# Performance work log

Measured on AMD Instinct MI355X. Metric: run time of the kernel, lower is better.

## Reference

```python
import jax, jax.numpy as jnp
import numpy as np

B, H, S, D = 4, 16, 2048, 64

def setup_inputs() -> dict:
    key = jax.random.key(0)
    kq, kk, kv = jax.random.split(key, 3)
    q = jax.random.normal(kq, (B, H, S, D), dtype=jnp.float32)
    k = jax.random.normal(kk, (B, H, S, D), dtype=jnp.float32)
    v = jax.random.normal(kv, (B, H, S, D), dtype=jnp.float32)
    # broadcastable causal mask: True = attend
    mask = jnp.tril(jnp.ones((S, S), dtype=bool))[None, None, :, :]
    return {"q": q, "k": k, "v": v, "mask": mask}

def reference(q, k, v, mask):
    # qk = einsum('... q d, ... k d -> ... q k'); mask -> -inf; softmax(qk/sqrt(d_k)); @ v
    scale = 1.0 / jnp.sqrt(jnp.asarray(q.shape[-1], q.dtype))
    scores = jnp.einsum('bhqd,bhkd->bhqk', q, k)
    scores = jnp.where(mask, scores, -jnp.inf) * scale  # -inf * scale stays -inf
    attn = jax.nn.softmax(scores, axis=-1)
    return jnp.einsum('bhqk,bhkd->bhqd', attn, v)
```

## Files before the change

kernel.cpp:

```cpp
#include <hip/hip_runtime.h>
#include <hip/hip_bf16.h>


#define SEQ 2048
#define HD  64

typedef __attribute__((ext_vector_type(8))) short short8;
typedef __attribute__((ext_vector_type(4))) float f32x4;

__device__ __forceinline__ short f2bf(float f) {
    union { float f; unsigned u; } x; x.f = f;
    unsigned r = x.u + 0x7fff + ((x.u >> 16) & 1);
    return (short)(r >> 16);
}

__device__ __forceinline__ short8 pack8(f32x4 a, f32x4 b, float s) {
    short8 t;
    t[0]=f2bf(a[0]*s); t[1]=f2bf(a[1]*s); t[2]=f2bf(a[2]*s); t[3]=f2bf(a[3]*s);
    t[4]=f2bf(b[0]*s); t[5]=f2bf(b[1]*s); t[6]=f2bf(b[2]*s); t[7]=f2bf(b[3]*s);
    return t;
}

#define KLD 72
#define VLD 40
#define ELD 68

__global__ __launch_bounds__(256, 4) void sdpa_kernel(
    const float* __restrict__ Q, const float* __restrict__ K,
    const float* __restrict__ V, float* __restrict__ O)
{
    __shared__ __align__(16) char smraw[4 * 16 * ELD * 4];
    short* Klds = (short*)smraw;
    short* Vlds = (short*)(smraw + 4608);

    const int bx = blockIdx.x;
    const int qt = 31 - (bx >> 6);
    const int bh = bx & 63;
    const int qbase = qt * 64;

    const int tid  = threadIdx.x;
    const int lane = tid & 63;
    const int w    = tid >> 6;
    const int g    = lane >> 4;
    const int r16  = lane & 15;
    const int wq   = qbase + w * 16;
    const int qrow = wq + r16;

    short8 qf[2];
    {
        const float* qp = Q + (size_t)(bh * SEQ + qrow) * HD + 8 * g;
        #pragma unroll
        for (int c = 0; c < 2; ++c) {
            f32x4 a = *(const f32x4*)(qp + c * 32);
            f32x4 b = *(const f32x4*)(qp + c * 32 + 4);
            qf[c] = pack8(a, b, 0.125f);
        }
    }

    f32x4 oacc[4] = {};
    float mrun = -1e30f, lrun = 0.0f;

    const int nkvb = (qbase + 64) >> 5;
    for (int kvb = 0; kvb < nkvb; ++kvb) {
        const int kvbase = kvb << 5;

        {
            const int kvo = tid >> 3;
            const int dc  = (tid & 7) * 8;
            const float* kp = K + (size_t)(bh * SEQ + kvbase + kvo) * HD + dc;
            f32x4 a = *(const f32x4*)kp;
            f32x4 b = *(const f32x4*)(kp + 4);
            const int p = 16 * ((kvo >> 2) & 1) + 4 * (kvo >> 3) + (kvo & 3);
            *(short8*)&Klds[p * KLD + dc] = pack8(a, b, 1.0f);
        }
        {
            const int kvo = tid & 31;
            const int dc  = (tid >> 5) * 8;
            const float* vp = V + (size_t)(bh * SEQ + kvbase + kvo) * HD + dc;
            f32x4 a = *(const f32x4*)vp;
            f32x4 b = *(const f32x4*)(vp + 4);
            Vlds[(dc + 0) * VLD + kvo] = f2bf(a[0]);
            Vlds[(dc + 1) * VLD + kvo] = f2bf(a[1]);
            Vlds[(dc + 2) * VLD + kvo] = f2bf(a[2]);
            Vlds[(dc + 3) * VLD + kvo] = f2bf(a[3]);
            Vlds[(dc + 4) * VLD + kvo] = f2bf(b[0]);
            Vlds[(dc + 5) * VLD + kvo] = f2bf(b[1]);
            Vlds[(dc + 6) * VLD + kvo] = f2bf(b[2]);
            Vlds[(dc + 7) * VLD + kvo] = f2bf(b[3]);
        }
        __syncthreads();

        if (kvbase <= wq + 15) {
            f32x4 sa[2];
            #pragma unroll
            for (int t = 0; t < 2; ++t) {
                f32x4 acc = {};
                #pragma unroll
                for (int c = 0; c < 2; ++c) {
                    short8 kf = *(const short8*)&Klds[(t * 16 + r16) * KLD + c * 32 + 8 * g];
                    acc = __builtin_amdgcn_mfma_f32_16x16x32_bf16(kf, qf[c], acc, 0, 0, 0);
                }
                sa[t] = acc;
            }
            if (kvbase + 31 > wq) {
                #pragma unroll
                for (int t = 0; t < 2; ++t)
                    #pragma unroll
                    for (int r = 0; r < 4; ++r) {
                        int kv = kvbase + 8 * g + 4 * t + r;
                        if (kv > qrow) sa[t][r] = -1e30f;
                    }
            }
            float mloc = sa[0][0];
            #pragma unroll
            for (int t = 0; t < 2; ++t)
                #pragma unroll
                for (int r = 0; r < 4; ++r) mloc = fmaxf(mloc, sa[t][r]);
            mloc = fmaxf(mloc, __shfl_xor(mloc, 16));
            mloc = fmaxf(mloc, __shfl_xor(mloc, 32));
            float mnew = fmaxf(mrun, mloc);
            float alpha = __expf(mrun - mnew);
            float ls = 0.0f;
            #pragma unroll
            for (int t = 0; t < 2; ++t)
                #pragma unroll
                for (int r = 0; r < 4; ++r) {
                    float p = __expf(sa[t][r] - mnew);
                    sa[t][r] = p; ls += p;
                }
            ls += __shfl_xor(ls, 16);
            ls += __shfl_xor(ls, 32);
            lrun = lrun * alpha + ls;
            mrun = mnew;
            short8 pf;
            pf[0] = f2bf(sa[0][0]); pf[1] = f2bf(sa[0][1]);
            pf[2] = f2bf(sa[0][2]); pf[3] = f2bf(sa[0][3]);
            pf[4] = f2bf(sa[1][0]); pf[5] = f2bf(sa[1][1]);
            pf[6] = f2bf(sa[1][2]); pf[7] = f2bf(sa[1][3]);
            #pragma unroll
            for (int dt = 0; dt < 4; ++dt) {
                f32x4 t2 = oacc[dt] * alpha;
                short8 vf = *(const short8*)&Vlds[(dt * 16 + r16) * VLD + 8 * g];
                oacc[dt] = __builtin_amdgcn_mfma_f32_16x16x32_bf16(vf, pf, t2, 0, 0, 0);
            }
        }
        __syncthreads();
    }

    const float inv = 1.0f / lrun;
    float* ep = (float*)smraw + w * (16 * ELD);
    #pragma unroll
    for (int dt = 0; dt < 4; ++dt)
        #pragma unroll
        for (int r = 0; r < 4; ++r)
            ep[r16 * ELD + dt * 16 + 4 * g + r] = oacc[dt][r] * inv;
    __syncthreads();

    const int qr = lane >> 2;
    const int cb = (lane & 3) * 16;
    const float* eprow = ep + qr * ELD + cb;
    float* op = O + (size_t)(bh * SEQ + wq + qr) * HD + cb;
    #pragma unroll
    for (int i = 0; i < 4; ++i)
        *(f32x4*)(op + 4 * i) = *(const f32x4*)(eprow + 4 * i);
}

extern "C" void kernel_launch(void* const* d_in, const int* in_sizes, int n_in,
                              void* d_out, int out_size, void* d_ws, size_t ws_size,
                              hipStream_t stream) {
    (void)in_sizes; (void)n_in; (void)out_size; (void)d_ws; (void)ws_size;
    const float* q = (const float*)d_in[0];
    const float* k = (const float*)d_in[1];
    const float* v = (const float*)d_in[2];
    float* o = (float*)d_out;
    sdpa_kernel<<<dim3(64 * 32), dim3(256), 0, stream>>>(q, k, v, o);
}
```

Measured before the change: 226.1 us.

## Enlarge attention tiles to 128 queries and 64 keys with swizzled LDS

Each workgroup now covers 128 query rows (two 16-row subtiles per wave) and 64-key blocks instead of 64/32. Every K and V fragment loaded from LDS therefore feeds two MFMAs, and there are fewer block iterations and barriers. LDS now uses XOR-swizzled layouts in place of padding, and bf16 conversion packs two values per word. Softmax uses exp2 with the log2e factor folded into the Q scale. The output is written straight from registers rather than staged through LDS. The cost is higher register pressure (launch bounds lowered to 2), half as many workgroups, and coarser causal-tile load imbalance.

```diff
diff --git a/kernel.cpp b/kernel.cpp
--- a/kernel.cpp
+++ b/kernel.cpp
@@ -1,5 +1,4 @@
 #include <hip/hip_runtime.h>
-#include <hip/hip_bf16.h>
 
 
 #define SEQ 2048
@@ -8,161 +7,205 @@
 typedef __attribute__((ext_vector_type(8))) short short8;
 typedef __attribute__((ext_vector_type(4))) float f32x4;
 
-__device__ __forceinline__ short f2bf(float f) {
+__device__ __forceinline__ unsigned f2bfu(float f) {
     union { float f; unsigned u; } x; x.f = f;
-    unsigned r = x.u + 0x7fff + ((x.u >> 16) & 1);
-    return (short)(r >> 16);
-}
-
-__device__ __forceinline__ short8 pack8(f32x4 a, f32x4 b, float s) {
-    short8 t;
-    t[0]=f2bf(a[0]*s); t[1]=f2bf(a[1]*s); t[2]=f2bf(a[2]*s); t[3]=f2bf(a[3]*s);
-    t[4]=f2bf(b[0]*s); t[5]=f2bf(b[1]*s); t[6]=f2bf(b[2]*s); t[7]=f2bf(b[3]*s);
-    return t;
-}
-
-#define KLD 72
-#define VLD 40
-#define ELD 68
-
-__global__ __launch_bounds__(256, 4) void sdpa_kernel(
+    return (x.u + 0x7fff + ((x.u >> 16) & 1)) >> 16;
+}
+__device__ __forceinline__ unsigned pk2(float lo, float hi) {
+    return f2bfu(lo) | (f2bfu(hi) << 16);
+}
+
+__global__ __launch_bounds__(256, 2) void sdpa_kernel(
     const float* __restrict__ Q, const float* __restrict__ K,
     const float* __restrict__ V, float* __restrict__ O)
 {
-    __shared__ __align__(16) char smraw[4 * 16 * ELD * 4];
-    short* Klds = (short*)smraw;
-    short* Vlds = (short*)(smraw + 4608);
+    __shared__ __align__(16) char smraw[16384];
+    char* Kl = smraw;
+    char* Vl = smraw + 8192;
 
     const int bx = blockIdx.x;
-    const int qt = 31 - (bx >> 6);
+    const int qt = 15 - (bx >> 6);
     const int bh = bx & 63;
-    const int qbase = qt * 64;
+    const int qbase = qt * 128;
 
     const int tid  = threadIdx.x;
     const int lane = tid & 63;
     const int w    = tid >> 6;
     const int g    = lane >> 4;
     const int r16  = lane & 15;
-    const int wq   = qbase + w * 16;
-    const int qrow = wq + r16;
-
-    short8 qf[2];
-    {
-        const float* qp = Q + (size_t)(bh * SEQ + qrow) * HD + 8 * g;
+    const int wq   = qbase + w * 32;
+
+    const size_t base = (size_t)bh * (SEQ * HD);
+
+    const float SC = 0.18033688011112042f;
+    short8 qf[2][2];
+    #pragma unroll
+    for (int qs = 0; qs < 2; ++qs) {
+        const float* qp = Q + base + (size_t)(wq + qs * 16 + r16) * HD + 8 * g;
         #pragma unroll
         for (int c = 0; c < 2; ++c) {
             f32x4 a = *(const f32x4*)(qp + c * 32);
             f32x4 b = *(const f32x4*)(qp + c * 32 + 4);
-            qf[c] = pack8(a, b, 0.125f);
+            union { short8 s; unsigned u[4]; } t;
+            t.u[0] = pk2(a[0] * SC, a[1] * SC);
+            t.u[1] = pk2(a[2] * SC, a[3] * SC);
+            t.u[2] = pk2(b[0] * SC, b[1] * SC);
+            t.u[3] = pk2(b[2] * SC, b[3] * SC);
+            qf[qs][c] = t.s;
         }
     }
 
-    f32x4 oacc[4] = {};
-    float mrun = -1e30f, lrun = 0.0f;
-
-    const int nkvb = (qbase + 64) >> 5;
+    f32x4 oacc[2][4] = {};
+    float mrun[2] = {-1e30f, -1e30f};
+    float lrun[2] = {0.0f, 0.0f};
+
+    const int k_kvo = tid >> 2;
+    const int k_o   = k_kvo & 31;
+    const int k_row = (k_kvo & 32) + 16 * ((k_o >> 2) & 1) + 4 * (k_o >> 3) + (k_o & 3);
+    const int k_dc  = (tid & 3) * 2;
+    const int v_kv0 = (tid & 31) * 2;
+    const int v_db  = (tid >> 5) * 8;
+
+    const int nkvb = (qbase + 128) >> 6;
     for (int kvb = 0; kvb < nkvb; ++kvb) {
-        const int kvbase = kvb << 5;
+        const int kvbase = kvb << 6;
 
         {
-            const int kvo = tid >> 3;
-            const int dc  = (tid & 7) * 8;
-            const float* kp = K + (size_t)(bh * SEQ + kvbase + kvo) * HD + dc;
-            f32x4 a = *(const f32x4*)kp;
-            f32x4 b = *(const f32x4*)(kp + 4);
-            const int p = 16 * ((kvo >> 2) & 1) + 4 * (kvo >> 3) + (kvo & 3);
-            *(short8*)&Klds[p * KLD + dc] = pack8(a, b, 1.0f);
+            const float* kp = K + base + (size_t)(kvbase + k_kvo) * HD + k_dc * 8;
+            f32x4 a0 = *(const f32x4*)(kp + 0);
+            f32x4 a1 = *(const f32x4*)(kp + 4);
+            f32x4 b0 = *(const f32x4*)(kp + 8);
+            f32x4 b1 = *(const f32x4*)(kp + 12);
+            union { short8 s; unsigned u[4]; } c0, c1;
+            c0.u[0] = pk2(a0[0], a0[1]); c0.u[1] = pk2(a0[2], a0[3]);
+            c0.u[2] = pk2(a1[0], a1[1]); c0.u[3] = pk2(a1[2], a1[3]);
+            c1.u[0] = pk2(b0[0], b0[1]); c1.u[1] = pk2(b0[2], b0[3]);
+            c1.u[2] = pk2(b1[0], b1[1]); c1.u[3] = pk2(b1[2], b1[3]);
+            const int r7 = k_row & 7;
+            *(short8*)(Kl + ((k_row * 8 + (k_dc ^ r7)) << 4))       = c0.s;
+            *(short8*)(Kl + ((k_row * 8 + ((k_dc + 1) ^ r7)) << 4)) = c1.s;
         }
         {
-            const int kvo = tid & 31;
-            const int dc  = (tid >> 5) * 8;
-            const float* vp = V + (size_t)(bh * SEQ + kvbase + kvo) * HD + dc;
-            f32x4 a = *(const f32x4*)vp;
-            f32x4 b = *(const f32x4*)(vp + 4);
-            Vlds[(dc + 0) * VLD + kvo] = f2bf(a[0]);
-            Vlds[(dc + 1) * VLD + kvo] = f2bf(a[1]);
-            Vlds[(dc + 2) * VLD + kvo] = f2bf(a[2]);
-            Vlds[(dc + 3) * VLD + kvo] = f2bf(a[3]);
-            Vlds[(dc + 4) * VLD + kvo] = f2bf(b[0]);
-            Vlds[(dc + 5) * VLD + kvo] = f2bf(b[1]);
-            Vlds[(dc + 6) * VLD + kvo] = f2bf(b[2]);
-            Vlds[(dc + 7) * VLD + kvo] = f2bf(b[3]);
+            const float* vp = V + base + (size_t)(kvbase + v_kv0) * HD + v_db;
+            f32x4 a0 = *(const f32x4*)(vp + 0);
+            f32x4 a1 = *(const f32x4*)(vp + 4);
+            f32x4 b0 = *(const f32x4*)(vp + HD);
+            f32x4 b1 = *(const f32x4*)(vp + HD + 4);
+            const int u  = v_kv0 >> 3;
+            const int wo = (v_kv0 & 7) * 2;
+            #pragma unroll
+            for (int i = 0; i < 4; ++i) {
+                const int d = v_db + i;
+                *(unsigned*)(Vl + ((d * 8 + (u ^ (d & 7))) << 4) + wo) = pk2(a0[i], b0[i]);
+            }
+            #pragma unroll
+            for (int i = 0; i < 4; ++i) {
+                const int d = v_db + 4 + i;
+                *(unsigned*)(Vl + ((d * 8 + (u ^ (d & 7))) << 4) + wo) = pk2(a1[i], b1[i]);
+            }
         }
         __syncthreads();
 
-        if (kvbase <= wq + 15) {
-            f32x4 sa[2];
-            #pragma unroll
-            for (int t = 0; t < 2; ++t) {
-                f32x4 acc = {};
-                #pragma unroll
-                for (int c = 0; c < 2; ++c) {
-                    short8 kf = *(const short8*)&Klds[(t * 16 + r16) * KLD + c * 32 + 8 * g];
-                    acc = __builtin_amdgcn_mfma_f32_16x16x32_bf16(kf, qf[c], acc, 0, 0, 0);
+        if (kvbase <= wq + 31) {
+            f32x4 sa[2][2][2];
+            #pragma unroll
+            for (int qs = 0; qs < 2; ++qs)
+                #pragma unroll
+                for (int c2 = 0; c2 < 2; ++c2)
+                    #pragma unroll
+                    for (int t = 0; t < 2; ++t)
+                        sa[qs][c2][t] = (f32x4){0.f, 0.f, 0.f, 0.f};
+            #pragma unroll
+            for (int c2 = 0; c2 < 2; ++c2)
+                #pragma unroll
+                for (int t = 0; t < 2; ++t)
+                    #pragma unroll
+                    for (int c = 0; c < 2; ++c) {
+                        const int row = c2 * 32 + t * 16 + r16;
+                        short8 kf = *(const short8*)(Kl + ((row * 8 + ((4 * c + g) ^ (row & 7))) << 4));
+                        sa[0][c2][t] = __builtin_amdgcn_mfma_f32_16x16x32_bf16(kf, qf[0][c], sa[0][c2][t], 0, 0, 0);
+                        sa[1][c2][t] = __builtin_amdgcn_mfma_f32_16x16x32_bf16(kf, qf[1][c], sa[1][c2][t], 0, 0, 0);
+                    }
+
+            #pragma unroll
+            for (int qs = 0; qs < 2; ++qs) {
+                const int q0 = wq + qs * 16;
+                const int qrow = q0 + r16;
+                if (kvbase + 63 > q0) {
+                    #pragma unroll
+                    for (int c2 = 0; c2 < 2; ++c2)
+                        #pragma unroll
+                        for (int t = 0; t < 2; ++t)
+                            #pragma unroll
+                            for (int r = 0; r < 4; ++r) {
+                                const int kv = kvbase + c2 * 32 + 8 * g + 4 * t + r;
+                                if (kv > qrow) sa[qs][c2][t][r] = -1e30f;
+                            }
                 }
-                sa[t] = acc;
-            }
-            if (kvbase + 31 > wq) {
-                #pragma unroll
-                for (int t = 0; t < 2; ++t)
-                    #pragma unroll
-                    for (int r = 0; r < 4; ++r) {
-                        int kv = kvbase + 8 * g + 4 * t + r;
-                        if (kv > qrow) sa[t][r] = -1e30f;
-                    }
-            }
-            float mloc = sa[0][0];
-            #pragma unroll
-            for (int t = 0; t < 2; ++t)
-                #pragma unroll
-                for (int r = 0; r < 4; ++r) mloc = fmaxf(mloc, sa[t][r]);
-            mloc = fmaxf(mloc, __shfl_xor(mloc, 16));
-            mloc = fmaxf(mloc, __shfl_xor(mloc, 32));
-            float mnew = fmaxf(mrun, mloc);
-            float alpha = __expf(mrun - mnew);
-            float ls = 0.0f;
-            #pragma unroll
-            for (int t = 0; t < 2; ++t)
-                #pragma unroll
-                for (int r = 0; r < 4; ++r) {
-                    float p = __expf(sa[t][r] - mnew);
-                    sa[t][r] = p; ls += p;
+                float mloc = sa[qs][0][0][0];
+                #pragma unroll
+                for (int c2 = 0; c2 < 2; ++c2)
+                    #pragma unroll
+                    for (int t = 0; t < 2; ++t)
+                        #pragma unroll
+                        for (int r = 0; r < 4; ++r)
+                            mloc = fmaxf(mloc, sa[qs][c2][t][r]);
+                mloc = fmaxf(mloc, __shfl_xor(mloc, 16));
+                mloc = fmaxf(mloc, __shfl_xor(mloc, 32));
+                const float mnew  = fmaxf(mrun[qs], mloc);
+                const float alpha = __builtin_amdgcn_exp2f(mrun[qs] - mnew);
+                float ls = 0.0f;
+                #pragma unroll
+                for (int c2 = 0; c2 < 2; ++c2)
+                    #pragma unroll
+                    for (int t = 0; t < 2; ++t)
+                        #pragma unroll
+                        for (int r = 0; r < 4; ++r) {
+                            const float p = __builtin_amdgcn_exp2f(sa[qs][c2][t][r] - mnew);
+                            sa[qs][c2][t][r] = p;
+                            ls += p;
+                        }
+                ls += __shfl_xor(ls, 16);
+                ls += __shfl_xor(ls, 32);
+                lrun[qs] = lrun[qs] * alpha + ls;
+                mrun[qs] = mnew;
+                #pragma unroll
+                for (int dt = 0; dt < 4; ++dt) oacc[qs][dt] *= alpha;
+            }
+
+            #pragma unroll
+            for (int c2 = 0; c2 < 2; ++c2) {
+                union { short8 s; unsigned u[4]; } pf0, pf1;
+                pf0.u[0] = pk2(sa[0][c2][0][0], sa[0][c2][0][1]);
+                pf0.u[1] = pk2(sa[0][c2][0][2], sa[0][c2][0][3]);
+                pf0.u[2] = pk2(sa[0][c2][1][0], sa[0][c2][1][1]);
+                pf0.u[3] = pk2(sa[0][c2][1][2], sa[0][c2][1][3]);
+                pf1.u[0] = pk2(sa[1][c2][0][0], sa[1][c2][0][1]);
+                pf1.u[1] = pk2(sa[1][c2][0][2], sa[1][c2][0][3]);
+                pf1.u[2] = pk2(sa[1][c2][1][0], sa[1][c2][1][1]);
+                pf1.u[3] = pk2(sa[1][c2][1][2], sa[1][c2][1][3]);
+                #pragma unroll
+                for (int dt = 0; dt < 4; ++dt) {
+                    const int row = dt * 16 + r16;
+                    short8 vf = *(const short8*)(Vl + ((row * 8 + ((c2 * 4 + g) ^ (row & 7))) << 4));
+                    oacc[0][dt] = __builtin_amdgcn_mfma_f32_16x16x32_bf16(vf, pf0.s, oacc[0][dt], 0, 0, 0);
+                    oacc[1][dt] = __builtin_amdgcn_mfma_f32_16x16x32_bf16(vf, pf1.s, oacc[1][dt], 0, 0, 0);
                 }
-            ls += __shfl_xor(ls, 16);
-            ls += __shfl_xor(ls, 32);
-            lrun = lrun * alpha + ls;
-            mrun = mnew;
-            short8 pf;
-            pf[0] = f2bf(sa[0][0]); pf[1] = f2bf(sa[0][1]);
-            pf[2] = f2bf(sa[0][2]); pf[3] = f2bf(sa[0][3]);
-            pf[4] = f2bf(sa[1][0]); pf[5] = f2bf(sa[1][1]);
-            pf[6] = f2bf(sa[1][2]); pf[7] = f2bf(sa[1][3]);
-            #pragma unroll
-            for (int dt = 0; dt < 4; ++dt) {
-                f32x4 t2 = oacc[dt] * alpha;
-                short8 vf = *(const short8*)&Vlds[(dt * 16 + r16) * VLD + 8 * g];
-                oacc[dt] = __builtin_amdgcn_mfma_f32_16x16x32_bf16(vf, pf, t2, 0, 0, 0);
             }
         }
         __syncthreads();
     }
 
-    const float inv = 1.0f / lrun;
-    float* ep = (float*)smraw + w * (16 * ELD);
     #pragma unroll
-    for (int dt = 0; dt < 4; ++dt)
+    for (int qs = 0; qs < 2; ++qs) {
+        const float inv = 1.0f / lrun[qs];
+        float* op = O + base + (size_t)(wq + qs * 16 + r16) * HD + 4 * g;
         #pragma unroll
-        for (int r = 0; r < 4; ++r)
-            ep[r16 * ELD + dt * 16 + 4 * g + r] = oacc[dt][r] * inv;
-    __syncthreads();
-
-    const int qr = lane >> 2;
-    const int cb = (lane & 3) * 16;
-    const float* eprow = ep + qr * ELD + cb;
-    float* op = O + (size_t)(bh * SEQ + wq + qr) * HD + cb;
-    #pragma unroll
-    for (int i = 0; i < 4; ++i)
-        *(f32x4*)(op + 4 * i) = *(const f32x4*)(eprow + 4 * i);
+        for (int dt = 0; dt < 4; ++dt) {
+            f32x4 vv = oacc[qs][dt] * inv;
+            *(f32x4*)(op + dt * 16) = vv;
+        }
+    }
 }
 
 extern "C" void kernel_launch(void* const* d_in, const int* in_sizes, int n_in,
@@ -173,5 +216,5 @@
     const float* k = (const float*)d_in[1];
     const float* v = (const float*)d_in[2];
     float* o = (float*)d_out;
-    sdpa_kernel<<<dim3(64 * 32), dim3(256), 0, stream>>>(q, k, v, o);
-}
+    sdpa_kernel<<<dim3(64 * 16), dim3(256), 0, stream>>>(q, k, v, o);
+}
```

Result: no change. 224.0 us (-0.9%).
